# Kernel optimization log

Hardware: AMD Instinct MI355X
Metric: run time of the kernel (lower is better)

The kernel has to match this reference:

```python
import jax, jax.numpy as jnp
import numpy as np

NCLASSES = 80
MAX_BOXES = 100
IOU_THR = 0.5
SCORE_THR = 0.0
NEG = -1e9


def arrange_bbox(xy, wh):
    # xy, wh: [1, H, W, 3, 2]
    H, W = xy.shape[1], xy.shape[2]
    gx, gy = jnp.meshgrid(jnp.arange(W), jnp.arange(H))  # 'xy' indexing, each [H, W]
    grid = jnp.stack([gx, gy], axis=-1)[:, :, None, :].astype(xy.dtype)  # [H, W, 1, 2]
    gsize = jnp.array([H, W], dtype=xy.dtype)  # TF divides last dim [x, y] by [H, W]
    xy = (xy + grid) / gsize
    return jnp.concatenate([xy - wh / 2, xy + wh / 2], axis=-1)  # [1,H,W,3,4]


def hard_nms(boxes, scores):
    # boxes: [N,4] (x1,y1,x2,y2); scores: [N]. Greedy NMS, fixed MAX_BOXES output.
    areas = (boxes[:, 2] - boxes[:, 0]) * (boxes[:, 3] - boxes[:, 1])  # [N]

    def step(sw, _):
        j = jnp.argmax(sw)
        s = sw[j]
        valid = s > SCORE_THR
        bj = boxes[j]
        iw = jnp.clip(jnp.minimum(boxes[:, 2], bj[2]) - jnp.maximum(boxes[:, 0], bj[0]), 0.0)
        ih = jnp.clip(jnp.minimum(boxes[:, 3], bj[3]) - jnp.maximum(boxes[:, 1], bj[1]), 0.0)
        inter = iw * ih
        iou = inter / (areas + areas[j] - inter)
        sw = jnp.where((iou > IOU_THR) & valid, NEG, sw)  # suppresses j itself too
        return sw, (jnp.where(valid, j, -1), jnp.where(valid, s, 0.0), valid)

    _, (sel_idx, sel_scores, valids) = jax.lax.scan(step, scores, None, length=MAX_BOXES)
    return sel_idx, sel_scores, valids


def decode(grid0, grid1, grid2, anchors_table):
    outs = (grid0, grid1, grid2)
    anch = (anchors_table[2], anchors_table[1], anchors_table[0])
    bbs, confs, probs = [], [], []
    for g, a in zip(outs, anch):
        xy, wh, obj, cp = jnp.split(g, [2, 4, 5], axis=-1)
        b = arrange_bbox(xy, jnp.exp(wh) * a)
        bbs.append(b.reshape(1, -1, 4))
        confs.append(obj.reshape(1, -1, 1))
        probs.append(cp.reshape(1, -1, NCLASSES))
    bbox = jnp.concatenate(bbs, axis=1).reshape(-1, 4)          # [N,4]
    conf = jnp.concatenate(confs, axis=1)[0, :, 0]              # [N]
    cp = jnp.concatenate(probs, axis=1)[0]                      # [N,C]
    cls_idx = jnp.argmax(cp, axis=-1)                           # [N]
    maxprob = jnp.max(cp, axis=-1)                              # [N]
    # TF code broadcasts conf[1,N,1]*maxprob[N] -> [N,N], then reduce_max over axis 1.
    # Mathematically: scores[i] = max_j conf[i]*maxprob[j] = max(conf*max(mp), conf*min(mp)).
    scores = jnp.maximum(conf * jnp.max(maxprob), conf * jnp.min(maxprob))
    return bbox, scores, cls_idx


def reference(grid0, grid1, grid2, anchors_table):
    bbox, scores, cls_idx = decode(grid0, grid1, grid2, anchors_table)
    sel_idx, sel_scores, valids = hard_nms(bbox, scores)
    safe = jnp.clip(sel_idx, 0)
    sel_boxes = jnp.where(valids[:, None], bbox[safe], 0.0)[None]      # [1,MAX,4]
    sel_scores = sel_scores[None]                                       # [1,MAX]
    sel_classes = jnp.where(valids, cls_idx[safe], 0)[None]            # [1,MAX]
    num_valid = jnp.sum(valids).astype(jnp.int32)[None]                # [1]
    return sel_boxes, sel_scores, sel_classes, num_valid


def setup_inputs() -> dict:
    key = jax.random.key(0)
    k0, k1, k2 = jax.random.split(key, 3)
    grid0 = jax.random.normal(k0, (1, 48, 48, 3, 85), jnp.float32)
    grid1 = jax.random.normal(k1, (1, 96, 96, 3, 85), jnp.float32)
    grid2 = jax.random.normal(k2, (1, 192, 192, 3, 85), jnp.float32)
    anchors = np.array([[[10, 13], [16, 30], [33, 23]],
                        [[30, 61], [62, 45], [59, 119]],
                        [[116, 90], [156, 198], [373, 326]]], np.float32) / 416.0
    return {"grid0": grid0, "grid1": grid1, "grid2": grid2,
            "anchors_table": jnp.asarray(anchors)}
```

## Files before the change

### kernel.cpp

```cpp
#include <hip/hip_runtime.h>
#include <hip/hip_bf16.h>
#include <math.h>


#define NCLS  80
#define MAXB  100
#define N0    6912
#define N1    27648
#define NTOT  145152
#define NTILE 2268
#define NB    4096
#define CAP   2048
#define CAPL  2048
#define CHUNK 256
#define NEGF  -3.402823466e38f
#define POSF   3.402823466e38f

#define WS_CONF 0
#define WS_SCAL (NTOT * 4)
#define WS_PART (WS_SCAL + 16)
#define WS_HIST (WS_PART + NTILE * 16)
#define WS_BINC (WS_HIST + 8 * NB * 4)
#define WS_SUF  (WS_BINC + NB * 4)
#define WS_META (WS_SUF + (NB + 2) * 4)
#define WS_CAND (WS_META + 16)

__device__ __forceinline__ int binOf(float s, float Smax) {
    int b = (int)((s / Smax) * (float)NB);
    return b > (NB - 1) ? (NB - 1) : b;
}
__device__ __forceinline__ float smaxOf(const float* scal) {
    float Mx = scal[0], Mn = scal[1], cmx = scal[2], cmn = scal[3];
    return fmaxf(fmaxf(cmx * Mx, cmx * Mn), fmaxf(cmn * Mx, cmn * Mn));
}
__device__ __forceinline__ float rdlane(float v, int l) {
    return __uint_as_float(__builtin_amdgcn_readlane(__float_as_uint(v), l));
}
__device__ __forceinline__ void decodeBox(int idx, const float* __restrict__ g0,
        const float* __restrict__ g1, const float* __restrict__ g2,
        const float* __restrict__ anch,
        float& x1, float& y1, float& x2, float& y2) {
    const float* g; int H, ar, j;
    if (idx < N0)           { g = g0; H = 48;  ar = 2; j = idx; }
    else if (idx < N0 + N1) { g = g1; H = 96;  ar = 1; j = idx - N0; }
    else                    { g = g2; H = 192; ar = 0; j = idx - N0 - N1; }
    const float* r = g + (size_t)j * 85;
    float tx = r[0], ty = r[1], tw = r[2], th = r[3];
    int cell = j / 3, a = j - cell * 3;
    int hh = cell / H, ww = cell - hh * H;
    float xc = (tx + (float)ww) / (float)H;
    float yc = (ty + (float)hh) / (float)H;
    float bw = expf(tw) * anch[ar * 6 + a * 2];
    float bh = expf(th) * anch[ar * 6 + a * 2 + 1];
    x1 = xc - bw * 0.5f; y1 = yc - bh * 0.5f;
    x2 = xc + bw * 0.5f; y2 = yc + bh * 0.5f;
}

__global__ __launch_bounds__(256) void k_decode(
        const float* __restrict__ g0, const float* __restrict__ g1,
        const float* __restrict__ g2, float* __restrict__ conf,
        float* __restrict__ part) {
    __shared__ float sm[5440];
    __shared__ float red[16];
    const int tid = threadIdx.x;
    const int tile = blockIdx.x;
    const float* p; int ibase, lt;
    if (tile < 108)      { p = g0; ibase = 0;       lt = tile; }
    else if (tile < 540) { p = g1; ibase = N0;      lt = tile - 108; }
    else                 { p = g2; ibase = N0 + N1; lt = tile - 540; }
    const float4* src = (const float4*)(p + (size_t)lt * 5440);
    for (int w = tid; w < 1360; w += 256) ((float4*)sm)[w] = src[w];
    __syncthreads();

    const int b = tid >> 2, pp = tid & 3;
    const float* row = sm + b * 85;
    float best = row[5 + pp * 20];
    #pragma unroll
    for (int k = 1; k < 20; k++) best = fmaxf(best, row[5 + pp * 20 + k]);
    best = fmaxf(best, __shfl_xor(best, 1));
    best = fmaxf(best, __shfl_xor(best, 2));
    float cmx = NEGF, cmn = POSF;
    if (pp == 0) {
        float obj = row[4];
        conf[ibase + lt * 64 + b] = obj;
        cmx = obj; cmn = obj;
    }
    float mpmax = best, mpmin = best;
    for (int off = 32; off; off >>= 1) {
        mpmax = fmaxf(mpmax, __shfl_down(mpmax, off));
        mpmin = fminf(mpmin, __shfl_down(mpmin, off));
        cmx   = fmaxf(cmx,   __shfl_down(cmx,   off));
        cmn   = fminf(cmn,   __shfl_down(cmn,   off));
    }
    const int lane = tid & 63, wid = tid >> 6;
    if (lane == 0) {
        red[wid * 4 + 0] = mpmax; red[wid * 4 + 1] = mpmin;
        red[wid * 4 + 2] = cmx;   red[wid * 4 + 3] = cmn;
    }
    __syncthreads();
    if (tid == 0) {
        float a0 = red[0], a1 = red[1], a2 = red[2], a3 = red[3];
        for (int w = 1; w < 4; w++) {
            a0 = fmaxf(a0, red[w * 4 + 0]); a1 = fminf(a1, red[w * 4 + 1]);
            a2 = fmaxf(a2, red[w * 4 + 2]); a3 = fminf(a3, red[w * 4 + 3]);
        }
        part[tile * 4 + 0] = a0; part[tile * 4 + 1] = a1;
        part[tile * 4 + 2] = a2; part[tile * 4 + 3] = a3;
    }
}

__global__ __launch_bounds__(256) void k_reduce(const float* __restrict__ part,
                                                float* __restrict__ scal) {
    __shared__ float red[16];
    const int tid = threadIdx.x;
    float a0 = NEGF, a1 = POSF, a2 = NEGF, a3 = POSF;
    for (int b = tid; b < NTILE; b += 256) {
        a0 = fmaxf(a0, part[b * 4 + 0]); a1 = fminf(a1, part[b * 4 + 1]);
        a2 = fmaxf(a2, part[b * 4 + 2]); a3 = fminf(a3, part[b * 4 + 3]);
    }
    for (int off = 32; off; off >>= 1) {
        a0 = fmaxf(a0, __shfl_down(a0, off)); a1 = fminf(a1, __shfl_down(a1, off));
        a2 = fmaxf(a2, __shfl_down(a2, off)); a3 = fminf(a3, __shfl_down(a3, off));
    }
    const int lane = tid & 63, wid = tid >> 6;
    if (lane == 0) {
        red[wid * 4 + 0] = a0; red[wid * 4 + 1] = a1;
        red[wid * 4 + 2] = a2; red[wid * 4 + 3] = a3;
    }
    __syncthreads();
    if (tid == 0) {
        for (int w = 1; w < 4; w++) {
            a0 = fmaxf(a0, red[w * 4 + 0]); a1 = fminf(a1, red[w * 4 + 1]);
            a2 = fmaxf(a2, red[w * 4 + 2]); a3 = fminf(a3, red[w * 4 + 3]);
        }
        scal[0] = a0; scal[1] = a1; scal[2] = a2; scal[3] = a3;
    }
}

__global__ __launch_bounds__(256) void k_hist(const float* __restrict__ conf,
                                              const float* __restrict__ scal,
                                              int* __restrict__ hist) {
    int i = blockIdx.x * 256 + threadIdx.x;
    float Mx = scal[0], Mn = scal[1];
    float Smax = smaxOf(scal);
    float c = conf[i];
    float s = fmaxf(c * Mx, c * Mn);
    if (s > 0.0f && Smax > 0.0f)
        atomicAdd(&hist[((blockIdx.x & 7) << 12) + binOf(s, Smax)], 1);
}

__global__ __launch_bounds__(1024) void k_thresh(const int* __restrict__ hist,
                                                 int* __restrict__ suf,
                                                 int* __restrict__ meta) {
    __shared__ int grp[1024];
    const int tid = threadIdx.x;
    int b0 = tid * 4;
    int h[4];
    #pragma unroll
    for (int q = 0; q < 4; q++) {
        int s = 0;
        #pragma unroll
        for (int sh = 0; sh < 8; sh++) s += hist[sh * NB + b0 + q];
        h[q] = s;
    }
    grp[tid] = h[0] + h[1] + h[2] + h[3];
    __syncthreads();
    for (int d = 1; d < 1024; d <<= 1) {
        int add = (tid + d < 1024) ? grp[tid + d] : 0;
        __syncthreads();
        grp[tid] += add;
        __syncthreads();
    }
    int gnext = (tid + 1 < 1024) ? grp[tid + 1] : 0;
    suf[b0 + 3] = gnext + h[3];
    suf[b0 + 2] = gnext + h[3] + h[2];
    suf[b0 + 1] = gnext + h[3] + h[2] + h[1];
    suf[b0 + 0] = gnext + h[3] + h[2] + h[1] + h[0];
    if (tid == 0) suf[NB] = 0;
    __syncthreads();
    if (tid == 0) {
        int L = 0, R = NB - 1, res = NB - 1;
        while (L <= R) {
            int m = (L + R) >> 1;
            if (suf[m] <= CAP) { res = m; R = m - 1; } else L = m + 1;
        }
        meta[0] = res;
    }
}

__global__ __launch_bounds__(256) void k_compact(
        const float* __restrict__ conf, const float* __restrict__ scal,
        const int* __restrict__ suf, const int* __restrict__ meta,
        int* __restrict__ binCtr, unsigned long long* __restrict__ cand) {
    int i = blockIdx.x * 256 + threadIdx.x;
    float Mx = scal[0], Mn = scal[1];
    float Smax = smaxOf(scal);
    float c = conf[i];
    float s = fmaxf(c * Mx, c * Mn);
    int lo = meta[0];
    if (s > 0.0f && Smax > 0.0f) {
        int b = binOf(s, Smax);
        if (b >= lo) {
            int pos = suf[b + 1] + atomicAdd(&binCtr[b], 1);
            if (pos < CAP)
                cand[pos] = ((unsigned long long)__float_as_uint(s) << 32)
                          | (unsigned long long)(~(unsigned)i);
        }
    }
}

__global__ __launch_bounds__(64) void k_nms(
        const float* __restrict__ g0, const float* __restrict__ g1,
        const float* __restrict__ g2, const float* __restrict__ anch,
        const float* __restrict__ conf, const float* __restrict__ scal,
        const int* __restrict__ suf, const int* __restrict__ meta,
        const unsigned long long* __restrict__ cand, float* __restrict__ out) {
    __shared__ unsigned long long keys[CAPL];
    __shared__ float selX1[MAXB], selY1[MAXB], selX2[MAXB], selY2[MAXB],
                     selA[MAXB], selS[MAXB];
    __shared__ int selIdx[MAXB];
    __shared__ int sh_cnt;

    const int lane = threadIdx.x;
    const float Mx = scal[0], Mn = scal[1];
    const float Smax = smaxOf(scal);
    const int loGlob = meta[0];
    int nsel = 0;
    int hi = NB;

    while (nsel < MAXB && hi > 0) {
        const bool fast = hi > loGlob;
        const int sufHi = suf[hi];
        int l;
        {
            int lb = fast ? loGlob : 0;
            int capHere = fast ? CHUNK : CAPL;
            int L = lb, R = hi - 1, res = hi - 1;
            while (L <= R) {
                int m = (L + R) >> 1;
                if (suf[m] - sufHi <= capHere) { res = m; R = m - 1; } else L = m + 1;
            }
            l = res;
        }
        int cnt;
        if (fast) {
            cnt = suf[l] - sufHi;
            for (int i = lane; i < cnt; i += 64) keys[i] = cand[sufHi + i];
        } else {
            if (lane == 0) sh_cnt = 0;
            __syncthreads();
            for (int i = lane; i < NTOT; i += 64) {
                float c = conf[i];
                float s = fmaxf(c * Mx, c * Mn);
                if (s > 0.0f) {
                    int b = binOf(s, Smax);
                    if (b >= l && b < hi) {
                        int pos = atomicAdd(&sh_cnt, 1);
                        if (pos < CAPL)
                            keys[pos] = ((unsigned long long)__float_as_uint(s) << 32)
                                      | (unsigned long long)(~(unsigned)i);
                    }
                }
            }
            __syncthreads();
            cnt = sh_cnt; if (cnt > CAPL) cnt = CAPL;
        }
        if (cnt > 0) {
            int n = 2; while (n < cnt) n <<= 1;
            for (int i = cnt + lane; i < n; i += 64) keys[i] = 0ULL;
            __syncthreads();
            for (int k = 2; k <= n; k <<= 1) {
                for (int j = k >> 1; j > 0; j >>= 1) {
                    int half = n >> 1;
                    for (int t = lane; t < half; t += 64) {
                        int i = ((t & ~(j - 1)) << 1) | (t & (j - 1));
                        int ixj = i | j;
                        unsigned long long ka = keys[i], kb = keys[ixj];
                        if ((ka < kb) == ((i & k) == 0)) { keys[i] = kb; keys[ixj] = ka; }
                    }
                    __syncthreads();
                }
            }
            for (int bpos = 0; bpos < cnt && nsel < MAXB; bpos += 64) {
                int t = bpos + lane;
                bool alive = (t < cnt);
                float x1 = 0.f, y1 = 0.f, x2 = 0.f, y2 = 0.f, area = 0.f, sc = 0.f;
                int idx = 0;
                if (alive) {
                    unsigned long long key = keys[t];
                    idx = (int)(~(unsigned)key);
                    sc = __uint_as_float((unsigned)(key >> 32));
                    decodeBox(idx, g0, g1, g2, anch, x1, y1, x2, y2);
                    area = (x2 - x1) * (y2 - y1);
                    for (int s2 = 0; s2 < nsel; s2++) {
                        float iw = fminf(x2, selX2[s2]) - fmaxf(x1, selX1[s2]);
                        float ih = fminf(y2, selY2[s2]) - fmaxf(y1, selY1[s2]);
                        iw = fmaxf(iw, 0.f); ih = fmaxf(ih, 0.f);
                        float inter = iw * ih;
                        if (inter / (area + selA[s2] - inter) > 0.5f) { alive = false; break; }
                    }
                }
                while (nsel < MAXB) {
                    unsigned long long bal = __ballot(alive);
                    if (!bal) break;
                    int w = __ffsll((unsigned long long)bal) - 1;
                    float wx1 = rdlane(x1, w), wy1 = rdlane(y1, w);
                    float wx2 = rdlane(x2, w), wy2 = rdlane(y2, w);
                    float wa  = rdlane(area, w);
                    if (lane == w) {
                        selX1[nsel] = x1; selY1[nsel] = y1;
                        selX2[nsel] = x2; selY2[nsel] = y2;
                        selA[nsel] = area; selS[nsel] = sc; selIdx[nsel] = idx;
                    }
                    if (alive) {
                        float iw = fminf(x2, wx2) - fmaxf(x1, wx1);
                        float ih = fminf(y2, wy2) - fmaxf(y1, wy1);
                        iw = fmaxf(iw, 0.f); ih = fmaxf(ih, 0.f);
                        float inter = iw * ih;
                        if (inter / (area + wa - inter) > 0.5f) alive = false;
                    }
                    nsel++;
                }
                __syncthreads();
            }
        }
        hi = l;
    }
    __syncthreads();

    for (int k = lane; k < MAXB; k += 64) {
        float b0 = 0.f, b1 = 0.f, b2 = 0.f, b3 = 0.f, sv = 0.f, cv = 0.f;
        if (k < nsel) {
            b0 = selX1[k]; b1 = selY1[k]; b2 = selX2[k]; b3 = selY2[k];
            sv = selS[k];
            int idx = selIdx[k];
            const float* g; int j;
            if (idx < N0)           { g = g0; j = idx; }
            else if (idx < N0 + N1) { g = g1; j = idx - N0; }
            else                    { g = g2; j = idx - N0 - N1; }
            const float* r = g + (size_t)j * 85 + 5;
            float best = r[0]; int c = 0;
            for (int q = 1; q < NCLS; q++) {
                float v = r[q];
                if (v > best) { best = v; c = q; }
            }
            cv = (float)c;
        }
        out[4 * k + 0] = b0; out[4 * k + 1] = b1;
        out[4 * k + 2] = b2; out[4 * k + 3] = b3;
        out[400 + k] = sv;
        out[500 + k] = cv;
    }
    if (lane == 0) out[600] = (float)nsel;
}

extern "C" void kernel_launch(void* const* d_in, const int* in_sizes, int n_in,
                              void* d_out, int out_size, void* d_ws, size_t ws_size,
                              hipStream_t stream) {
    const float* g0   = (const float*)d_in[0];
    const float* g1   = (const float*)d_in[1];
    const float* g2   = (const float*)d_in[2];
    const float* anch = (const float*)d_in[3];
    char* ws = (char*)d_ws;
    float* conf  = (float*)(ws + WS_CONF);
    float* scal  = (float*)(ws + WS_SCAL);
    float* part  = (float*)(ws + WS_PART);
    int*   hist  = (int*)(ws + WS_HIST);
    int*   binc  = (int*)(ws + WS_BINC);
    int*   suf   = (int*)(ws + WS_SUF);
    int*   meta  = (int*)(ws + WS_META);
    unsigned long long* cand = (unsigned long long*)(ws + WS_CAND);
    float* out   = (float*)d_out;

    hipMemsetAsync(ws + WS_HIST, 0, 9 * NB * 4, stream);
    k_decode <<<NTILE, 256, 0, stream>>>(g0, g1, g2, conf, part);
    k_reduce <<<1, 256, 0, stream>>>(part, scal);
    k_hist   <<<NTOT / 256, 256, 0, stream>>>(conf, scal, hist);
    k_thresh <<<1, 1024, 0, stream>>>(hist, suf, meta);
    k_compact<<<NTOT / 256, 256, 0, stream>>>(conf, scal, suf, meta, binc, cand);
    k_nms    <<<1, 64, 0, stream>>>(g0, g1, g2, anch, conf, scal, suf, meta, cand, out);
}
```

Baseline: 168.8 us.

## Fuse reduce and threshold kernels into predecessors via last-block atomic counters

The single-block reduce kernel moves into the tail of k_decode, and the threshold/suffix-scan kernel moves into the tail of k_hist. In each case the last block to finish, found through an atomic counter, does the work, which removes two kernel launches and their launch gaps. The suffix scan now runs with 256 threads handling 16 bins each instead of 1024 threads handling 4. The NMS class argmax is also fully unrolled into a register array. In exchange, the fusion adds threadfence and atomic overhead to every block, and the final reduction runs in only one block.

```diff
diff --git a/kernel.cpp b/kernel.cpp
--- a/kernel.cpp
+++ b/kernel.cpp
@@ -9,6 +9,7 @@
 #define N1    27648
 #define NTOT  145152
 #define NTILE 2268
+#define NHB   567
 #define NB    4096
 #define CAP   2048
 #define CAPL  2048
@@ -19,11 +20,13 @@
 #define WS_CONF 0
 #define WS_SCAL (NTOT * 4)
 #define WS_PART (WS_SCAL + 16)
-#define WS_HIST (WS_PART + NTILE * 16)
-#define WS_BINC (WS_HIST + 8 * NB * 4)
-#define WS_SUF  (WS_BINC + NB * 4)
+#define WS_SUF  (WS_PART + NTILE * 16)
 #define WS_META (WS_SUF + (NB + 2) * 4)
 #define WS_CAND (WS_META + 16)
+#define WS_HIST (WS_CAND + CAP * 8)
+#define WS_BINC (WS_HIST + 8 * NB * 4)
+#define WS_CTR  (WS_BINC + NB * 4)
+#define WS_ZEROSZ (8 * NB * 4 + NB * 4 + 16)
 
 __device__ __forceinline__ int binOf(float s, float Smax) {
     int b = (int)((s / Smax) * (float)NB);
@@ -59,9 +62,11 @@
 __global__ __launch_bounds__(256) void k_decode(
         const float* __restrict__ g0, const float* __restrict__ g1,
         const float* __restrict__ g2, float* __restrict__ conf,
-        float* __restrict__ part) {
+        float* __restrict__ part, float* __restrict__ scal,
+        int* __restrict__ ctr) {
     __shared__ float sm[5440];
     __shared__ float red[16];
+    __shared__ int sh_last;
     const int tid = threadIdx.x;
     const int tile = blockIdx.x;
     const float* p; int ibase, lt;
@@ -106,23 +111,22 @@
         }
         part[tile * 4 + 0] = a0; part[tile * 4 + 1] = a1;
         part[tile * 4 + 2] = a2; part[tile * 4 + 3] = a3;
-    }
-}
-
-__global__ __launch_bounds__(256) void k_reduce(const float* __restrict__ part,
-                                                float* __restrict__ scal) {
-    __shared__ float red[16];
-    const int tid = threadIdx.x;
+        __threadfence();
+        sh_last = (atomicAdd(&ctr[0], 1) == NTILE - 1);
+    }
+    __syncthreads();
+    if (!sh_last) return;
+    __threadfence();
     float a0 = NEGF, a1 = POSF, a2 = NEGF, a3 = POSF;
-    for (int b = tid; b < NTILE; b += 256) {
-        a0 = fmaxf(a0, part[b * 4 + 0]); a1 = fminf(a1, part[b * 4 + 1]);
-        a2 = fmaxf(a2, part[b * 4 + 2]); a3 = fminf(a3, part[b * 4 + 3]);
+    for (int t = tid; t < NTILE; t += 256) {
+        float4 p4 = ((const float4*)part)[t];
+        a0 = fmaxf(a0, p4.x); a1 = fminf(a1, p4.y);
+        a2 = fmaxf(a2, p4.z); a3 = fminf(a3, p4.w);
     }
     for (int off = 32; off; off >>= 1) {
         a0 = fmaxf(a0, __shfl_down(a0, off)); a1 = fminf(a1, __shfl_down(a1, off));
         a2 = fmaxf(a2, __shfl_down(a2, off)); a3 = fminf(a3, __shfl_down(a3, off));
     }
-    const int lane = tid & 63, wid = tid >> 6;
     if (lane == 0) {
         red[wid * 4 + 0] = a0; red[wid * 4 + 1] = a1;
         red[wid * 4 + 2] = a2; red[wid * 4 + 3] = a3;
@@ -137,45 +141,47 @@
     }
 }
 
-__global__ __launch_bounds__(256) void k_hist(const float* __restrict__ conf,
-                                              const float* __restrict__ scal,
-                                              int* __restrict__ hist) {
-    int i = blockIdx.x * 256 + threadIdx.x;
-    float Mx = scal[0], Mn = scal[1];
-    float Smax = smaxOf(scal);
-    float c = conf[i];
-    float s = fmaxf(c * Mx, c * Mn);
-    if (s > 0.0f && Smax > 0.0f)
-        atomicAdd(&hist[((blockIdx.x & 7) << 12) + binOf(s, Smax)], 1);
-}
-
-__global__ __launch_bounds__(1024) void k_thresh(const int* __restrict__ hist,
-                                                 int* __restrict__ suf,
-                                                 int* __restrict__ meta) {
-    __shared__ int grp[1024];
+__global__ __launch_bounds__(256) void k_hist(
+        const float* __restrict__ conf, const float* __restrict__ scal,
+        int* __restrict__ hist, int* __restrict__ ctr,
+        int* __restrict__ suf, int* __restrict__ meta) {
     const int tid = threadIdx.x;
-    int b0 = tid * 4;
-    int h[4];
+    __shared__ int sh_last;
+    __shared__ int grp[256];
+    {
+        int i = blockIdx.x * 256 + tid;
+        float Mx = scal[0], Mn = scal[1];
+        float Smax = smaxOf(scal);
+        float c = conf[i];
+        float s = fmaxf(c * Mx, c * Mn);
+        if (s > 0.0f && Smax > 0.0f)
+            atomicAdd(&hist[((blockIdx.x & 7) << 12) + binOf(s, Smax)], 1);
+    }
+    __threadfence();
+    if (tid == 0) sh_last = (atomicAdd(&ctr[1], 1) == NHB - 1);
+    __syncthreads();
+    if (!sh_last) return;
+    __threadfence();
+    int b0 = tid * 16;
+    int h[16], tot = 0;
     #pragma unroll
-    for (int q = 0; q < 4; q++) {
-        int s = 0;
+    for (int q = 0; q < 16; q++) {
+        int ss = 0;
         #pragma unroll
-        for (int sh = 0; sh < 8; sh++) s += hist[sh * NB + b0 + q];
-        h[q] = s;
-    }
-    grp[tid] = h[0] + h[1] + h[2] + h[3];
-    __syncthreads();
-    for (int d = 1; d < 1024; d <<= 1) {
-        int add = (tid + d < 1024) ? grp[tid + d] : 0;
+        for (int sh = 0; sh < 8; sh++) ss += hist[sh * NB + b0 + q];
+        h[q] = ss; tot += ss;
+    }
+    grp[tid] = tot;
+    __syncthreads();
+    for (int d = 1; d < 256; d <<= 1) {
+        int add = (tid + d < 256) ? grp[tid + d] : 0;
         __syncthreads();
         grp[tid] += add;
         __syncthreads();
     }
-    int gnext = (tid + 1 < 1024) ? grp[tid + 1] : 0;
-    suf[b0 + 3] = gnext + h[3];
-    suf[b0 + 2] = gnext + h[3] + h[2];
-    suf[b0 + 1] = gnext + h[3] + h[2] + h[1];
-    suf[b0 + 0] = gnext + h[3] + h[2] + h[1] + h[0];
+    int run = (tid + 1 < 256) ? grp[tid + 1] : 0;
+    #pragma unroll
+    for (int q = 15; q >= 0; q--) { run += h[q]; suf[b0 + q] = run; }
     if (tid == 0) suf[NB] = 0;
     __syncthreads();
     if (tid == 0) {
@@ -339,11 +345,13 @@
             else if (idx < N0 + N1) { g = g1; j = idx - N0; }
             else                    { g = g2; j = idx - N0 - N1; }
             const float* r = g + (size_t)j * 85 + 5;
-            float best = r[0]; int c = 0;
-            for (int q = 1; q < NCLS; q++) {
-                float v = r[q];
-                if (v > best) { best = v; c = q; }
-            }
+            float v[NCLS];
+            #pragma unroll
+            for (int q = 0; q < NCLS; q++) v[q] = r[q];
+            float best = v[0]; int c = 0;
+            #pragma unroll
+            for (int q = 1; q < NCLS; q++)
+                if (v[q] > best) { best = v[q]; c = q; }
             cv = (float)c;
         }
         out[4 * k + 0] = b0; out[4 * k + 1] = b1;
@@ -365,18 +373,17 @@
     float* conf  = (float*)(ws + WS_CONF);
     float* scal  = (float*)(ws + WS_SCAL);
     float* part  = (float*)(ws + WS_PART);
-    int*   hist  = (int*)(ws + WS_HIST);
-    int*   binc  = (int*)(ws + WS_BINC);
     int*   suf   = (int*)(ws + WS_SUF);
     int*   meta  = (int*)(ws + WS_META);
     unsigned long long* cand = (unsigned long long*)(ws + WS_CAND);
+    int*   hist  = (int*)(ws + WS_HIST);
+    int*   binc  = (int*)(ws + WS_BINC);
+    int*   ctr   = (int*)(ws + WS_CTR);
     float* out   = (float*)d_out;
 
-    hipMemsetAsync(ws + WS_HIST, 0, 9 * NB * 4, stream);
-    k_decode <<<NTILE, 256, 0, stream>>>(g0, g1, g2, conf, part);
-    k_reduce <<<1, 256, 0, stream>>>(part, scal);
-    k_hist   <<<NTOT / 256, 256, 0, stream>>>(conf, scal, hist);
-    k_thresh <<<1, 1024, 0, stream>>>(hist, suf, meta);
-    k_compact<<<NTOT / 256, 256, 0, stream>>>(conf, scal, suf, meta, binc, cand);
+    hipMemsetAsync(ws + WS_HIST, 0, WS_ZEROSZ, stream);
+    k_decode <<<NTILE, 256, 0, stream>>>(g0, g1, g2, conf, part, scal, ctr);
+    k_hist   <<<NHB, 256, 0, stream>>>(conf, scal, hist, ctr, suf, meta);
+    k_compact<<<NHB, 256, 0, stream>>>(conf, scal, suf, meta, binc, cand);
     k_nms    <<<1, 64, 0, stream>>>(g0, g1, g2, anch, conf, scal, suf, meta, cand, out);
 }
```

Measured after the change: 232.9 us. 1.38x slower.
